# Performance work log

Hardware: AMD Instinct MI355X
Metric: run time of the kernel (lower is better)

The kernel has to match this reference:

```python
import jax, jax.numpy as jnp
import numpy as np

B, T, D, H = 8, 4096, 512, 512


def setup_inputs() -> dict:
    key = jax.random.key(0)
    k1, k2, k3, k4, k5, k6 = jax.random.split(key, 6)
    lim = 1.0 / np.sqrt(D)
    return {
        "x": jax.random.normal(k1, (B, T, D), dtype=jnp.float32),
        "h_0": jax.random.normal(k2, (B, 1, H), dtype=jnp.float32),
        "W_z": jax.random.uniform(k3, (H, D), jnp.float32, -lim, lim),
        "b_z": jax.random.uniform(k4, (H,), jnp.float32, -lim, lim),
        "W_h": jax.random.uniform(k5, (H, D), jnp.float32, -lim, lim),
        "b_h": jax.random.uniform(k6, (H,), jnp.float32, -lim, lim),
    }


def reference(x, h_0, W_z, b_z, W_h, b_h):
    # z_t = sigmoid(W_z x_t), h~_t = tanh(W_h x_t)
    z = jax.nn.sigmoid(jnp.einsum('btd,hd->bth', x, W_z) + b_z)  # (B,T,H)
    h_tilde = jnp.tanh(jnp.einsum('btd,hd->bth', x, W_h) + b_h)  # (B,T,H)
    a = 1.0 - z            # multiplicative coeffs
    b = z * h_tilde        # additive terms (b[:,0] handled as h0 carry)

    # linear recurrence h_t = a_t * h_{t-1} + b_t, h_0 given
    def scan_fn(h_prev, ab):
        a_t, b_t = ab
        h_t = a_t * h_prev + b_t
        return h_t, h_t

    a_t = jnp.swapaxes(a, 0, 1)  # (T,B,H)
    b_t = jnp.swapaxes(b, 0, 1)  # (T,B,H)
    _, hs = jax.lax.scan(scan_fn, h_0[:, 0, :], (a_t, b_t))
    return jnp.swapaxes(hs, 0, 1)  # (B,T,H)
```

## Files before the change

### kernel.cpp

```cpp
#include <hip/hip_runtime.h>

constexpr int Bn = 8, Tn = 4096, Dn = 512, Hn = 512;
constexpr int Mn = Bn * Tn;
constexpr int CH = 64, NC = Tn / CH;

typedef __attribute__((ext_vector_type(8))) short s8v;
typedef __attribute__((ext_vector_type(4))) float f4v;
typedef __attribute__((ext_vector_type(8))) _Float16 h8v;
typedef unsigned short ushort_t;

typedef __attribute__((address_space(1))) const void gv_t;
typedef __attribute__((address_space(3))) void lv_t;

__device__ __forceinline__ short f2bf(float f) {
  unsigned u = __float_as_uint(f);
  u = (u + 0x7fffu + ((u >> 16) & 1u)) >> 16;
  return (short)u;
}

__global__ __launch_bounds__(256) void convert_x(
    const float* __restrict__ X, ushort_t* __restrict__ Xb) {
  int lb = blockIdx.x, tid = threadIdx.x;
  const float* tsrc = X + ((size_t)(lb >> 4) * 128) * Dn + (lb & 15) * 32;
#pragma unroll
  for (int p = 0; p < 2; p++) {
    int idx = tid + p * 256;
    int r = idx >> 2, k8 = idx & 3;
    const float4* sv = reinterpret_cast<const float4*>(tsrc + (size_t)r * Dn + k8 * 8);
    float4 f0 = sv[0], f1 = sv[1];
    s8v v;
    v[0] = f2bf(f0.x); v[1] = f2bf(f0.y); v[2] = f2bf(f0.z); v[3] = f2bf(f0.w);
    v[4] = f2bf(f1.x); v[5] = f2bf(f1.y); v[6] = f2bf(f1.z); v[7] = f2bf(f1.w);
    int c = (r >> 4) * 64 + k8 * 16 + (r & 15);
    *reinterpret_cast<s8v*>(&Xb[((size_t)lb * 512 + c) * 8]) = v;
  }
}

__global__ __launch_bounds__(256) void convert_w(
    const float* __restrict__ Wz, const float* __restrict__ Wh,
    ushort_t* __restrict__ Wzb, ushort_t* __restrict__ Whb) {
  int bx = blockIdx.x, tid = threadIdx.x;
  const float* src;
  ushort_t* dst;
  int lb;
  if (bx < 64) { src = Wz; dst = Wzb; lb = bx; }
  else         { src = Wh; dst = Whb; lb = bx - 64; }
  const float* tsrc = src + ((size_t)(lb >> 4) * 128) * Dn + (lb & 15) * 32;
#pragma unroll
  for (int p = 0; p < 2; p++) {
    int idx = tid + p * 256;
    int r = idx >> 2, k8 = idx & 3;
    const float4* sv = reinterpret_cast<const float4*>(tsrc + (size_t)r * Dn + k8 * 8);
    float4 f0 = sv[0], f1 = sv[1];
    s8v v;
    v[0] = f2bf(f0.x); v[1] = f2bf(f0.y); v[2] = f2bf(f0.z); v[3] = f2bf(f0.w);
    v[4] = f2bf(f1.x); v[5] = f2bf(f1.y); v[6] = f2bf(f1.z); v[7] = f2bf(f1.w);
    int c = (r >> 4) * 64 + k8 * 16 + (r & 15);
    *reinterpret_cast<s8v*>(&dst[((size_t)lb * 512 + c) * 8]) = v;
  }
}

__global__ __launch_bounds__(512, 2) void gemm_act(
    const ushort_t* __restrict__ Xb, const ushort_t* __restrict__ Wzb,
    const ushort_t* __restrict__ Whb,
    const float* __restrict__ bzp, const float* __restrict__ bhp,
    h8v* __restrict__ cab, float* __restrict__ cA, float* __restrict__ cB) {
  __shared__ __align__(16) ushort_t lds[32 * 2048];

  int tid = threadIdx.x, lane = tid & 63, wid = tid >> 6;

  int o = blockIdx.x;
  int loc = o >> 3;
  int mt = (o & 7) * 8 + (loc >> 3);
  int p = loc & 7;

#pragma unroll
  for (int q = 0; q < 16; q++) {
    int r = q * 2 + (wid >> 2);
    int kt = r & 15;
    const ushort_t* wsrc = (r >= 16 ? Whb : Wzb);
    const ushort_t* s = wsrc + ((size_t)((p >> 1) * 16 + kt)) * 4096 + (p & 1) * 2048 + (tid & 255) * 8;
    __builtin_amdgcn_global_load_lds((gv_t*)s, (lv_t*)(lds + r * 2048 + (tid & 255) * 8), 16, 0, 0);
  }

  f4v accz[4][4], acch[4][4];
#pragma unroll
  for (int i = 0; i < 4; i++)
#pragma unroll
    for (int j = 0; j < 4; j++) {
      accz[i][j] = (f4v){0.f, 0.f, 0.f, 0.f};
      acch[i][j] = (f4v){0.f, 0.f, 0.f, 0.f};
    }

  int rw = mt * 8 + wid;
  int rt = rw >> 1, half = rw & 1;
  const ushort_t* xb = Xb + (size_t)rt * 16 * 4096;

  __syncthreads();

  auto ldW = [&](int kt, s8v* bzf, s8v* bhf) {
#pragma unroll
    for (int j = 0; j < 4; j++) {
      bzf[j] = *reinterpret_cast<const s8v*>(lds + (size_t)kt * 2048 + (j * 64 + lane) * 8);
      bhf[j] = *reinterpret_cast<const s8v*>(lds + (size_t)(16 + kt) * 2048 + (j * 64 + lane) * 8);
    }
  };
  auto mfmaStep = [&](s8v* af, s8v* bzf, s8v* bhf) {
    __builtin_amdgcn_s_setprio(1);
#pragma unroll
    for (int i = 0; i < 4; i++)
#pragma unroll
      for (int j = 0; j < 4; j++) {
        accz[i][j] = __builtin_amdgcn_mfma_f32_16x16x32_bf16(af[i], bzf[j], accz[i][j], 0, 0, 0);
        acch[i][j] = __builtin_amdgcn_mfma_f32_16x16x32_bf16(af[i], bhf[j], acch[i][j], 0, 0, 0);
      }
    __builtin_amdgcn_s_setprio(0);
  };

  s8v afA[4], afB[4];
#pragma unroll
  for (int i = 0; i < 4; i++)
    afA[i] = *reinterpret_cast<const s8v*>(xb + ((half * 4 + i) * 64 + lane) * 8);

#pragma unroll
  for (int kp = 0; kp < 8; kp++) {
    int k0 = 2 * kp;
#pragma unroll
    for (int i = 0; i < 4; i++)
      afB[i] = *reinterpret_cast<const s8v*>(xb + (size_t)(k0 + 1) * 4096 + ((half * 4 + i) * 64 + lane) * 8);
    s8v bz0[4], bh0[4];
    ldW(k0, bz0, bh0);
    mfmaStep(afA, bz0, bh0);
    if (k0 + 2 < 16) {
#pragma unroll
      for (int i = 0; i < 4; i++)
        afA[i] = *reinterpret_cast<const s8v*>(xb + (size_t)(k0 + 2) * 4096 + ((half * 4 + i) * 64 + lane) * 8);
    }
    s8v bz1[4], bh1[4];
    ldW(k0 + 1, bz1, bh1);
    mfmaStep(afB, bz1, bh1);
  }

  int R = rw, Cc = p;
  size_t base = (size_t)(R * 8 + Cc) * 1024;
  float bzv[4], bhv[4];
#pragma unroll
  for (int j = 0; j < 4; j++) {
    int h = p * 64 + j * 16 + (lane & 15);
    bzv[j] = bzp[h];
    bhv[j] = bhp[h];
  }
  float QA[4][4], QB[4][4];
#pragma unroll
  for (int i = 0; i < 4; i++)
#pragma unroll
    for (int j = 0; j < 4; j++) {
      h8v g;
      float Pa = 1.f, Pb = 0.f;
#pragma unroll
      for (int q = 0; q < 4; q++) {
        float z = 1.f / (1.f + __expf(-(accz[i][j][q] + bzv[j])));
        float e = __expf(2.f * (acch[i][j][q] + bhv[j]));
        float th = 1.f - 2.f / (e + 1.f);
        g[q] = (_Float16)(1.f - z);
        g[4 + q] = (_Float16)(z * th);
        float a = (float)g[q], b = (float)g[4 + q];
        Pa = a * Pa;
        Pb = a * Pb + b;
      }
      cab[base + (size_t)((i * 4 + j) * 64 + lane)] = g;
      QA[i][j] = Pa;
      QB[i][j] = Pb;
    }

#pragma unroll
  for (int j = 0; j < 4; j++) {
    float A = 1.f, Bv = 0.f;
#pragma unroll
    for (int i = 0; i < 4; i++) {
      float a = QA[i][j], b = QB[i][j];
      float ap = __shfl_xor(a, 16), bp = __shfl_xor(b, 16);
      bool hi = (lane & 16) != 0;
      float af_ = hi ? ap : a, bf_ = hi ? bp : b;
      float as_ = hi ? a : ap, bs_ = hi ? b : bp;
      a = as_ * af_; b = as_ * bf_ + bs_;
      ap = __shfl_xor(a, 32); bp = __shfl_xor(b, 32);
      bool hi2 = (lane & 32) != 0;
      af_ = hi2 ? ap : a; bf_ = hi2 ? bp : b;
      as_ = hi2 ? a : ap; bs_ = hi2 ? b : bp;
      a = as_ * af_; b = as_ * bf_ + bs_;
      Bv = a * Bv + b;
      A = a * A;
    }
    if (lane < 16) {
      int h = p * 64 + j * 16 + lane;
      cA[(size_t)R * Hn + h] = A;
      cB[(size_t)R * Hn + h] = Bv;
    }
  }
}

__global__ __launch_bounds__(256) void scan_heads(
    const float* __restrict__ cA, const float* __restrict__ cB,
    const float* __restrict__ h0p, float* __restrict__ hst) {
  int gid = blockIdx.x * 256 + threadIdx.x;
  int b = gid >> 9, h = gid & 511;
  float hr = h0p[(size_t)b * Hn + h];
#pragma unroll 8
  for (int c = 0; c < NC; c++) {
    size_t o = (size_t)(b * NC + c) * Hn + h;
    hst[o] = hr;
    hr = fmaf(cA[o], hr, cB[o]);
  }
}

__global__ __launch_bounds__(256) void scan_apply(
    const h8v* __restrict__ cab, const float* __restrict__ hst,
    float* __restrict__ out) {
  int h = blockIdx.y * 256 + threadIdx.x;
  int R = blockIdx.x;
  int hl = h & 63, Cc = h >> 6;
  size_t base = (size_t)(R * 8 + Cc) * 1024 + (size_t)(hl >> 4) * 64 + (hl & 15);
  float hr = hst[(size_t)R * Hn + h];
  size_t ob = (size_t)R * 64 * Hn + h;
#pragma unroll
  for (int i = 0; i < 4; i++)
#pragma unroll
    for (int p = 0; p < 4; p++) {
      h8v g = cab[base + i * 256 + p * 16];
#pragma unroll
      for (int q = 0; q < 4; q++) {
        hr = fmaf((float)g[q], hr, (float)g[4 + q]);
        out[ob + (size_t)(i * 16 + p * 4 + q) * Hn] = hr;
      }
    }
}

extern "C" void kernel_launch(void* const* d_in, const int* in_sizes, int n_in,
                              void* d_out, int out_size, void* d_ws, size_t ws_size,
                              hipStream_t stream) {
  const float* X   = (const float*)d_in[0];
  const float* h0p = (const float*)d_in[1];
  const float* Wz  = (const float*)d_in[2];
  const float* bz  = (const float*)d_in[3];
  const float* Wh  = (const float*)d_in[4];
  const float* bh  = (const float*)d_in[5];
  float* out = (float*)d_out;

  char* ws = (char*)d_ws;
  ushort_t* Xb  = (ushort_t*)ws;
  ushort_t* Wzb = Xb + (size_t)Mn * Dn;
  ushort_t* Whb = Wzb + (size_t)Hn * Dn;
  h8v* cab      = (h8v*)(Whb + (size_t)Hn * Dn);
  float* cA     = (float*)(cab + (size_t)Mn * Hn / 4);
  float* cB     = cA + (size_t)Bn * NC * Hn;
  float* hst    = cB + (size_t)Bn * NC * Hn;

  convert_x<<<dim3(4096), 256, 0, stream>>>(X, Xb);
  convert_w<<<dim3(128), 256, 0, stream>>>(Wz, Wh, Wzb, Whb);

  gemm_act<<<dim3(512), 512, 0, stream>>>(Xb, Wzb, Whb, bz, bh, cab, cA, cB);

  scan_heads<<<dim3(Bn * Hn / 256), 256, 0, stream>>>(cA, cB, h0p, hst);
  scan_apply<<<dim3(Mn / 64, Hn / 256), 256, 0, stream>>>(cab, hst, out);
}
```

Measured before the change: 95.66 us.

## Fuse x bf16 conversion into GEMM and loop two M-tiles per block

Removes the separate convert_x pass and its bf16 workspace. The GEMM now reads fp32 x straight from global memory and converts it to bf16 in registers with v_cvt_pk_bf16_f32. Each block loops over two M tiles so the W tiles loaded into LDS are reused twice, which halves the grid to 256 blocks. The trade-off is that the GEMM reads twice as many bytes of x per fragment, and with 256 blocks of 512 threads at launch_bounds 2 per CU, occupancy is roughly one block per CU.

```diff
diff --git a/kernel.cpp b/kernel.cpp
--- a/kernel.cpp
+++ b/kernel.cpp
@@ -16,24 +16,6 @@
   unsigned u = __float_as_uint(f);
   u = (u + 0x7fffu + ((u >> 16) & 1u)) >> 16;
   return (short)u;
-}
-
-__global__ __launch_bounds__(256) void convert_x(
-    const float* __restrict__ X, ushort_t* __restrict__ Xb) {
-  int lb = blockIdx.x, tid = threadIdx.x;
-  const float* tsrc = X + ((size_t)(lb >> 4) * 128) * Dn + (lb & 15) * 32;
-#pragma unroll
-  for (int p = 0; p < 2; p++) {
-    int idx = tid + p * 256;
-    int r = idx >> 2, k8 = idx & 3;
-    const float4* sv = reinterpret_cast<const float4*>(tsrc + (size_t)r * Dn + k8 * 8);
-    float4 f0 = sv[0], f1 = sv[1];
-    s8v v;
-    v[0] = f2bf(f0.x); v[1] = f2bf(f0.y); v[2] = f2bf(f0.z); v[3] = f2bf(f0.w);
-    v[4] = f2bf(f1.x); v[5] = f2bf(f1.y); v[6] = f2bf(f1.z); v[7] = f2bf(f1.w);
-    int c = (r >> 4) * 64 + k8 * 16 + (r & 15);
-    *reinterpret_cast<s8v*>(&Xb[((size_t)lb * 512 + c) * 8]) = v;
-  }
 }
 
 __global__ __launch_bounds__(256) void convert_w(
@@ -61,18 +43,16 @@
 }
 
 __global__ __launch_bounds__(512, 2) void gemm_act(
-    const ushort_t* __restrict__ Xb, const ushort_t* __restrict__ Wzb,
+    const float* __restrict__ X, const ushort_t* __restrict__ Wzb,
     const ushort_t* __restrict__ Whb,
     const float* __restrict__ bzp, const float* __restrict__ bhp,
     h8v* __restrict__ cab, float* __restrict__ cA, float* __restrict__ cB) {
   __shared__ __align__(16) ushort_t lds[32 * 2048];
 
   int tid = threadIdx.x, lane = tid & 63, wid = tid >> 6;
-
   int o = blockIdx.x;
-  int loc = o >> 3;
-  int mt = (o & 7) * 8 + (loc >> 3);
-  int p = loc & 7;
+  int p = o & 7;
+  int mtp = o >> 3;
 
 #pragma unroll
   for (int q = 0; q < 16; q++) {
@@ -82,20 +62,6 @@
     const ushort_t* s = wsrc + ((size_t)((p >> 1) * 16 + kt)) * 4096 + (p & 1) * 2048 + (tid & 255) * 8;
     __builtin_amdgcn_global_load_lds((gv_t*)s, (lv_t*)(lds + r * 2048 + (tid & 255) * 8), 16, 0, 0);
   }
-
-  f4v accz[4][4], acch[4][4];
-#pragma unroll
-  for (int i = 0; i < 4; i++)
-#pragma unroll
-    for (int j = 0; j < 4; j++) {
-      accz[i][j] = (f4v){0.f, 0.f, 0.f, 0.f};
-      acch[i][j] = (f4v){0.f, 0.f, 0.f, 0.f};
-    }
-
-  int rw = mt * 8 + wid;
-  int rt = rw >> 1, half = rw & 1;
-  const ushort_t* xb = Xb + (size_t)rt * 16 * 4096;
-
   __syncthreads();
 
   auto ldW = [&](int kt, s8v* bzf, s8v* bhf) {
@@ -105,97 +71,115 @@
       bhf[j] = *reinterpret_cast<const s8v*>(lds + (size_t)(16 + kt) * 2048 + (j * 64 + lane) * 8);
     }
   };
-  auto mfmaStep = [&](s8v* af, s8v* bzf, s8v* bhf) {
-    __builtin_amdgcn_s_setprio(1);
+  auto cvtFrag = [&](const float4& a, const float4& b) -> s8v {
+    union { unsigned u[4]; s8v v; } r;
+    asm("v_cvt_pk_bf16_f32 %0, %1, %2" : "=v"(r.u[0]) : "v"(a.x), "v"(a.y));
+    asm("v_cvt_pk_bf16_f32 %0, %1, %2" : "=v"(r.u[1]) : "v"(a.z), "v"(a.w));
+    asm("v_cvt_pk_bf16_f32 %0, %1, %2" : "=v"(r.u[2]) : "v"(b.x), "v"(b.y));
+    asm("v_cvt_pk_bf16_f32 %0, %1, %2" : "=v"(r.u[3]) : "v"(b.z), "v"(b.w));
+    return r.v;
+  };
+
+  for (int m2 = 0; m2 < 2; m2++) {
+    int mt = mtp * 2 + m2;
+    int rw = mt * 8 + wid;
+    const float* Xp = X + (size_t)(rw * 64 + (lane & 15)) * Dn + (lane >> 4) * 8;
+
+    auto loadX = [&](int kt, float4* xf) {
+#pragma unroll
+      for (int i = 0; i < 4; i++) {
+        const float4* si = reinterpret_cast<const float4*>(Xp + (size_t)i * 16 * Dn + kt * 32);
+        xf[2 * i] = si[0];
+        xf[2 * i + 1] = si[1];
+      }
+    };
+
+    f4v accz[4][4], acch[4][4];
 #pragma unroll
     for (int i = 0; i < 4; i++)
 #pragma unroll
       for (int j = 0; j < 4; j++) {
-        accz[i][j] = __builtin_amdgcn_mfma_f32_16x16x32_bf16(af[i], bzf[j], accz[i][j], 0, 0, 0);
-        acch[i][j] = __builtin_amdgcn_mfma_f32_16x16x32_bf16(af[i], bhf[j], acch[i][j], 0, 0, 0);
-      }
-    __builtin_amdgcn_s_setprio(0);
-  };
-
-  s8v afA[4], afB[4];
-#pragma unroll
-  for (int i = 0; i < 4; i++)
-    afA[i] = *reinterpret_cast<const s8v*>(xb + ((half * 4 + i) * 64 + lane) * 8);
-
-#pragma unroll
-  for (int kp = 0; kp < 8; kp++) {
-    int k0 = 2 * kp;
+        accz[i][j] = (f4v){0.f, 0.f, 0.f, 0.f};
+        acch[i][j] = (f4v){0.f, 0.f, 0.f, 0.f};
+      }
+
+    float4 xf[8];
+    loadX(0, xf);
+#pragma unroll
+    for (int kt = 0; kt < 16; kt++) {
+      s8v af[4];
+#pragma unroll
+      for (int i = 0; i < 4; i++) af[i] = cvtFrag(xf[2 * i], xf[2 * i + 1]);
+      if (kt < 15) loadX(kt + 1, xf);
+      s8v bzf[4], bhf[4];
+      ldW(kt, bzf, bhf);
+      __builtin_amdgcn_s_setprio(1);
+#pragma unroll
+      for (int i = 0; i < 4; i++)
+#pragma unroll
+        for (int j = 0; j < 4; j++) {
+          accz[i][j] = __builtin_amdgcn_mfma_f32_16x16x32_bf16(af[i], bzf[j], accz[i][j], 0, 0, 0);
+          acch[i][j] = __builtin_amdgcn_mfma_f32_16x16x32_bf16(af[i], bhf[j], acch[i][j], 0, 0, 0);
+        }
+      __builtin_amdgcn_s_setprio(0);
+    }
+
+    int R = rw, Cc = p;
+    size_t base = (size_t)(R * 8 + Cc) * 1024;
+    float bzv[4], bhv[4];
+#pragma unroll
+    for (int j = 0; j < 4; j++) {
+      int h = p * 64 + j * 16 + (lane & 15);
+      bzv[j] = bzp[h];
+      bhv[j] = bhp[h];
+    }
+    float QA[4][4], QB[4][4];
 #pragma unroll
     for (int i = 0; i < 4; i++)
-      afB[i] = *reinterpret_cast<const s8v*>(xb + (size_t)(k0 + 1) * 4096 + ((half * 4 + i) * 64 + lane) * 8);
-    s8v bz0[4], bh0[4];
-    ldW(k0, bz0, bh0);
-    mfmaStep(afA, bz0, bh0);
-    if (k0 + 2 < 16) {
-#pragma unroll
-      for (int i = 0; i < 4; i++)
-        afA[i] = *reinterpret_cast<const s8v*>(xb + (size_t)(k0 + 2) * 4096 + ((half * 4 + i) * 64 + lane) * 8);
-    }
-    s8v bz1[4], bh1[4];
-    ldW(k0 + 1, bz1, bh1);
-    mfmaStep(afB, bz1, bh1);
-  }
-
-  int R = rw, Cc = p;
-  size_t base = (size_t)(R * 8 + Cc) * 1024;
-  float bzv[4], bhv[4];
-#pragma unroll
-  for (int j = 0; j < 4; j++) {
-    int h = p * 64 + j * 16 + (lane & 15);
-    bzv[j] = bzp[h];
-    bhv[j] = bhp[h];
-  }
-  float QA[4][4], QB[4][4];
-#pragma unroll
-  for (int i = 0; i < 4; i++)
+#pragma unroll
+      for (int j = 0; j < 4; j++) {
+        h8v g;
+        float Pa = 1.f, Pb = 0.f;
+#pragma unroll
+        for (int q = 0; q < 4; q++) {
+          float z = 1.f / (1.f + __expf(-(accz[i][j][q] + bzv[j])));
+          float e = __expf(2.f * (acch[i][j][q] + bhv[j]));
+          float th = 1.f - 2.f / (e + 1.f);
+          g[q] = (_Float16)(1.f - z);
+          g[4 + q] = (_Float16)(z * th);
+          float a = (float)g[q], b = (float)g[4 + q];
+          Pa = a * Pa;
+          Pb = a * Pb + b;
+        }
+        cab[base + (size_t)((i * 4 + j) * 64 + lane)] = g;
+        QA[i][j] = Pa;
+        QB[i][j] = Pb;
+      }
+
 #pragma unroll
     for (int j = 0; j < 4; j++) {
-      h8v g;
-      float Pa = 1.f, Pb = 0.f;
-#pragma unroll
-      for (int q = 0; q < 4; q++) {
-        float z = 1.f / (1.f + __expf(-(accz[i][j][q] + bzv[j])));
-        float e = __expf(2.f * (acch[i][j][q] + bhv[j]));
-        float th = 1.f - 2.f / (e + 1.f);
-        g[q] = (_Float16)(1.f - z);
-        g[4 + q] = (_Float16)(z * th);
-        float a = (float)g[q], b = (float)g[4 + q];
-        Pa = a * Pa;
-        Pb = a * Pb + b;
-      }
-      cab[base + (size_t)((i * 4 + j) * 64 + lane)] = g;
-      QA[i][j] = Pa;
-      QB[i][j] = Pb;
-    }
-
-#pragma unroll
-  for (int j = 0; j < 4; j++) {
-    float A = 1.f, Bv = 0.f;
-#pragma unroll
-    for (int i = 0; i < 4; i++) {
-      float a = QA[i][j], b = QB[i][j];
-      float ap = __shfl_xor(a, 16), bp = __shfl_xor(b, 16);
-      bool hi = (lane & 16) != 0;
-      float af_ = hi ? ap : a, bf_ = hi ? bp : b;
-      float as_ = hi ? a : ap, bs_ = hi ? b : bp;
-      a = as_ * af_; b = as_ * bf_ + bs_;
-      ap = __shfl_xor(a, 32); bp = __shfl_xor(b, 32);
-      bool hi2 = (lane & 32) != 0;
-      af_ = hi2 ? ap : a; bf_ = hi2 ? bp : b;
-      as_ = hi2 ? a : ap; bs_ = hi2 ? b : bp;
-      a = as_ * af_; b = as_ * bf_ + bs_;
-      Bv = a * Bv + b;
-      A = a * A;
-    }
-    if (lane < 16) {
-      int h = p * 64 + j * 16 + lane;
-      cA[(size_t)R * Hn + h] = A;
-      cB[(size_t)R * Hn + h] = Bv;
+      float A = 1.f, Bv = 0.f;
+#pragma unroll
+      for (int i = 0; i < 4; i++) {
+        float a = QA[i][j], b = QB[i][j];
+        float ap = __shfl_xor(a, 16), bp = __shfl_xor(b, 16);
+        bool hi = (lane & 16) != 0;
+        float af_ = hi ? ap : a, bf_ = hi ? bp : b;
+        float as_ = hi ? a : ap, bs_ = hi ? b : bp;
+        a = as_ * af_; b = as_ * bf_ + bs_;
+        ap = __shfl_xor(a, 32); bp = __shfl_xor(b, 32);
+        bool hi2 = (lane & 32) != 0;
+        af_ = hi2 ? ap : a; bf_ = hi2 ? bp : b;
+        as_ = hi2 ? a : ap; bs_ = hi2 ? b : bp;
+        a = as_ * af_; b = as_ * bf_ + bs_;
+        Bv = a * Bv + b;
+        A = a * A;
+      }
+      if (lane < 16) {
+        int h = p * 64 + j * 16 + lane;
+        cA[(size_t)R * Hn + h] = A;
+        cB[(size_t)R * Hn + h] = Bv;
+      }
     }
   }
 }
@@ -248,18 +232,16 @@
   float* out = (float*)d_out;
 
   char* ws = (char*)d_ws;
-  ushort_t* Xb  = (ushort_t*)ws;
-  ushort_t* Wzb = Xb + (size_t)Mn * Dn;
+  ushort_t* Wzb = (ushort_t*)ws;
   ushort_t* Whb = Wzb + (size_t)Hn * Dn;
   h8v* cab      = (h8v*)(Whb + (size_t)Hn * Dn);
   float* cA     = (float*)(cab + (size_t)Mn * Hn / 4);
   float* cB     = cA + (size_t)Bn * NC * Hn;
   float* hst    = cB + (size_t)Bn * NC * Hn;
 
-  convert_x<<<dim3(4096), 256, 0, stream>>>(X, Xb);
   convert_w<<<dim3(128), 256, 0, stream>>>(Wz, Wh, Wzb, Whb);
 
-  gemm_act<<<dim3(512), 512, 0, stream>>>(Xb, Wzb, Whb, bz, bh, cab, cA, cB);
+  gemm_act<<<dim3(256), 512, 0, stream>>>(X, Wzb, Whb, bz, bh, cab, cA, cB);
 
   scan_heads<<<dim3(Bn * Hn / 256), 256, 0, stream>>>(cA, cB, h0p, hst);
   scan_apply<<<dim3(Mn / 64, Hn / 256), 256, 0, stream>>>(cab, hst, out);
```

Measured after the change: 134.3 us. 40.4% more time.

## Split GEMM block across 16 waves, halving per-wave N tile

Applied to the files above, without the earlier changes.

Grows the gemm_act block from 8 to 16 waves. Each pair of waves now shares a 64-row M strip and splits the 64 columns into two 32-column halves, which cuts per-wave accumulators from 32 to 16 MFMA tiles and lowers register pressure. W staging into LDS is spread over 1024 threads and the s_setprio hints are removed. Each X fragment is now loaded from global twice (once per column-half wave), so global X traffic doubles. That extra traffic is traded for more waves in flight to hide latency.

```diff
diff --git a/kernel.cpp b/kernel.cpp
--- a/kernel.cpp
+++ b/kernel.cpp
@@ -60,107 +60,100 @@
   }
 }
 
-__global__ __launch_bounds__(512, 2) void gemm_act(
+__global__ __launch_bounds__(1024, 4) void gemm_act(
     const ushort_t* __restrict__ Xb, const ushort_t* __restrict__ Wzb,
     const ushort_t* __restrict__ Whb,
     const float* __restrict__ bzp, const float* __restrict__ bhp,
     h8v* __restrict__ cab, float* __restrict__ cA, float* __restrict__ cB) {
-  __shared__ __align__(16) ushort_t lds[32 * 2048];
+  __shared__ __align__(16) ushort_t lds[65536];
 
   int tid = threadIdx.x, lane = tid & 63, wid = tid >> 6;
+  int wr = wid >> 1, wc = wid & 1;
 
   int o = blockIdx.x;
   int loc = o >> 3;
   int mt = (o & 7) * 8 + (loc >> 3);
   int p = loc & 7;
 
-#pragma unroll
-  for (int q = 0; q < 16; q++) {
-    int r = q * 2 + (wid >> 2);
-    int kt = r & 15;
-    const ushort_t* wsrc = (r >= 16 ? Whb : Wzb);
-    const ushort_t* s = wsrc + ((size_t)((p >> 1) * 16 + kt)) * 4096 + (p & 1) * 2048 + (tid & 255) * 8;
-    __builtin_amdgcn_global_load_lds((gv_t*)s, (lv_t*)(lds + r * 2048 + (tid & 255) * 8), 16, 0, 0);
-  }
-
-  f4v accz[4][4], acch[4][4];
+  const ushort_t* wzp = Wzb + ((size_t)(p >> 1) * 16) * 4096 + (p & 1) * 2048;
+  const ushort_t* whp = Whb + ((size_t)(p >> 1) * 16) * 4096 + (p & 1) * 2048;
+#pragma unroll
+  for (int q = 0; q < 8; q++) {
+    int idx = q * 1024 + tid;
+    int r = idx >> 8, cc = idx & 255;
+    const ushort_t* src = (r < 16 ? wzp + (size_t)r * 4096
+                                  : whp + (size_t)(r - 16) * 4096) + cc * 8;
+    __builtin_amdgcn_global_load_lds((gv_t*)src, (lv_t*)(lds + idx * 8), 16, 0, 0);
+  }
+
+  f4v accz[4][2], acch[4][2];
 #pragma unroll
   for (int i = 0; i < 4; i++)
 #pragma unroll
-    for (int j = 0; j < 4; j++) {
-      accz[i][j] = (f4v){0.f, 0.f, 0.f, 0.f};
-      acch[i][j] = (f4v){0.f, 0.f, 0.f, 0.f};
-    }
-
-  int rw = mt * 8 + wid;
+    for (int jj = 0; jj < 2; jj++) {
+      accz[i][jj] = (f4v){0.f, 0.f, 0.f, 0.f};
+      acch[i][jj] = (f4v){0.f, 0.f, 0.f, 0.f};
+    }
+
+  int rw = mt * 8 + wr;
   int rt = rw >> 1, half = rw & 1;
-  const ushort_t* xb = Xb + (size_t)rt * 16 * 4096;
+  const s8v* xs = reinterpret_cast<const s8v*>(Xb) + (size_t)rt * 16 * 512 + (half * 4) * 64 + lane;
+  const ushort_t* lz = lds;
+  const ushort_t* lh = lds + 32768;
+  int cb0 = (wc * 2) * 64 + lane;
 
   __syncthreads();
 
-  auto ldW = [&](int kt, s8v* bzf, s8v* bhf) {
-#pragma unroll
-    for (int j = 0; j < 4; j++) {
-      bzf[j] = *reinterpret_cast<const s8v*>(lds + (size_t)kt * 2048 + (j * 64 + lane) * 8);
-      bhf[j] = *reinterpret_cast<const s8v*>(lds + (size_t)(16 + kt) * 2048 + (j * 64 + lane) * 8);
-    }
+  auto ldX = [&](s8v* A, int kt) {
+#pragma unroll
+    for (int i = 0; i < 4; i++) A[i] = xs[kt * 512 + i * 64];
   };
-  auto mfmaStep = [&](s8v* af, s8v* bzf, s8v* bhf) {
-    __builtin_amdgcn_s_setprio(1);
+  auto step = [&](int kt, s8v* A) {
+    s8v bz[2], bh[2];
+#pragma unroll
+    for (int jj = 0; jj < 2; jj++) {
+      bz[jj] = *reinterpret_cast<const s8v*>(lz + (size_t)kt * 2048 + (size_t)(cb0 + jj * 64) * 8);
+      bh[jj] = *reinterpret_cast<const s8v*>(lh + (size_t)kt * 2048 + (size_t)(cb0 + jj * 64) * 8);
+    }
 #pragma unroll
     for (int i = 0; i < 4; i++)
 #pragma unroll
-      for (int j = 0; j < 4; j++) {
-        accz[i][j] = __builtin_amdgcn_mfma_f32_16x16x32_bf16(af[i], bzf[j], accz[i][j], 0, 0, 0);
-        acch[i][j] = __builtin_amdgcn_mfma_f32_16x16x32_bf16(af[i], bhf[j], acch[i][j], 0, 0, 0);
+      for (int jj = 0; jj < 2; jj++) {
+        accz[i][jj] = __builtin_amdgcn_mfma_f32_16x16x32_bf16(A[i], bz[jj], accz[i][jj], 0, 0, 0);
+        acch[i][jj] = __builtin_amdgcn_mfma_f32_16x16x32_bf16(A[i], bh[jj], acch[i][jj], 0, 0, 0);
       }
-    __builtin_amdgcn_s_setprio(0);
   };
 
-  s8v afA[4], afB[4];
-#pragma unroll
-  for (int i = 0; i < 4; i++)
-    afA[i] = *reinterpret_cast<const s8v*>(xb + ((half * 4 + i) * 64 + lane) * 8);
-
+  s8v A0[4], A1[4];
+  ldX(A0, 0); ldX(A1, 1);
 #pragma unroll
   for (int kp = 0; kp < 8; kp++) {
-    int k0 = 2 * kp;
-#pragma unroll
-    for (int i = 0; i < 4; i++)
-      afB[i] = *reinterpret_cast<const s8v*>(xb + (size_t)(k0 + 1) * 4096 + ((half * 4 + i) * 64 + lane) * 8);
-    s8v bz0[4], bh0[4];
-    ldW(k0, bz0, bh0);
-    mfmaStep(afA, bz0, bh0);
-    if (k0 + 2 < 16) {
-#pragma unroll
-      for (int i = 0; i < 4; i++)
-        afA[i] = *reinterpret_cast<const s8v*>(xb + (size_t)(k0 + 2) * 4096 + ((half * 4 + i) * 64 + lane) * 8);
-    }
-    s8v bz1[4], bh1[4];
-    ldW(k0 + 1, bz1, bh1);
-    mfmaStep(afB, bz1, bh1);
+    step(2 * kp, A0);
+    if (kp < 7) ldX(A0, 2 * kp + 2);
+    step(2 * kp + 1, A1);
+    if (kp < 7) ldX(A1, 2 * kp + 3);
   }
 
   int R = rw, Cc = p;
   size_t base = (size_t)(R * 8 + Cc) * 1024;
-  float bzv[4], bhv[4];
-#pragma unroll
-  for (int j = 0; j < 4; j++) {
-    int h = p * 64 + j * 16 + (lane & 15);
-    bzv[j] = bzp[h];
-    bhv[j] = bhp[h];
-  }
-  float QA[4][4], QB[4][4];
+  float bzv[2], bhv[2];
+#pragma unroll
+  for (int jj = 0; jj < 2; jj++) {
+    int h = p * 64 + (wc * 2 + jj) * 16 + (lane & 15);
+    bzv[jj] = bzp[h];
+    bhv[jj] = bhp[h];
+  }
+  float QA[4][2], QB[4][2];
 #pragma unroll
   for (int i = 0; i < 4; i++)
 #pragma unroll
-    for (int j = 0; j < 4; j++) {
+    for (int jj = 0; jj < 2; jj++) {
       h8v g;
       float Pa = 1.f, Pb = 0.f;
 #pragma unroll
       for (int q = 0; q < 4; q++) {
-        float z = 1.f / (1.f + __expf(-(accz[i][j][q] + bzv[j])));
-        float e = __expf(2.f * (acch[i][j][q] + bhv[j]));
+        float z = 1.f / (1.f + __expf(-(accz[i][jj][q] + bzv[jj])));
+        float e = __expf(2.f * (acch[i][jj][q] + bhv[jj]));
         float th = 1.f - 2.f / (e + 1.f);
         g[q] = (_Float16)(1.f - z);
         g[4 + q] = (_Float16)(z * th);
@@ -168,17 +161,17 @@
         Pa = a * Pa;
         Pb = a * Pb + b;
       }
-      cab[base + (size_t)((i * 4 + j) * 64 + lane)] = g;
-      QA[i][j] = Pa;
-      QB[i][j] = Pb;
-    }
-
-#pragma unroll
-  for (int j = 0; j < 4; j++) {
+      cab[base + (size_t)((i * 4 + wc * 2 + jj) * 64 + lane)] = g;
+      QA[i][jj] = Pa;
+      QB[i][jj] = Pb;
+    }
+
+#pragma unroll
+  for (int jj = 0; jj < 2; jj++) {
     float A = 1.f, Bv = 0.f;
 #pragma unroll
     for (int i = 0; i < 4; i++) {
-      float a = QA[i][j], b = QB[i][j];
+      float a = QA[i][jj], b = QB[i][jj];
       float ap = __shfl_xor(a, 16), bp = __shfl_xor(b, 16);
       bool hi = (lane & 16) != 0;
       float af_ = hi ? ap : a, bf_ = hi ? bp : b;
@@ -193,7 +186,7 @@
       A = a * A;
     }
     if (lane < 16) {
-      int h = p * 64 + j * 16 + lane;
+      int h = p * 64 + (wc * 2 + jj) * 16 + lane;
       cA[(size_t)R * Hn + h] = A;
       cB[(size_t)R * Hn + h] = Bv;
     }
@@ -259,7 +252,7 @@
   convert_x<<<dim3(4096), 256, 0, stream>>>(X, Xb);
   convert_w<<<dim3(128), 256, 0, stream>>>(Wz, Wh, Wzb, Whb);
 
-  gemm_act<<<dim3(512), 512, 0, stream>>>(Xb, Wzb, Whb, bz, bh, cab, cA, cB);
+  gemm_act<<<dim3(512), 1024, 0, stream>>>(Xb, Wzb, Whb, bz, bh, cab, cA, cB);
 
   scan_heads<<<dim3(Bn * Hn / 256), 256, 0, stream>>>(cA, cB, h0p, hst);
   scan_apply<<<dim3(Mn / 64, Hn / 256), 256, 0, stream>>>(cab, hst, out);
```

Result: slower. 101.8 us (+6.4%).

## Restructure gemm_act into a double-buffered LDS-staged 2D block tiling

Applied to the files above, without the earlier changes.

The fused gate GEMM now tiles each workgroup as a 256-row by 128-column block and stages both X and W tiles through LDS. Staging uses double-buffered global_load_lds, with explicit waitcnt and barriers so the next K-step loads while the current one runs MFMAs. Previously each wave streamed its own X rows straight from global memory and only W was cached in LDS. Each wave now computes either the z or the h projection for a 128x64 sub-tile, and the partner results are swapped through LDS before the activation and chunk-scan epilogue. The aim is better reuse of X and W and more overlap of loads with compute, at the cost of extra barriers and an LDS exchange of accumulators.

```diff
diff --git a/kernel.cpp b/kernel.cpp
--- a/kernel.cpp
+++ b/kernel.cpp
@@ -65,88 +65,121 @@
     const ushort_t* __restrict__ Whb,
     const float* __restrict__ bzp, const float* __restrict__ bhp,
     h8v* __restrict__ cab, float* __restrict__ cA, float* __restrict__ cB) {
-  __shared__ __align__(16) ushort_t lds[32 * 2048];
+  __shared__ __align__(16) ushort_t lds[65536];
 
   int tid = threadIdx.x, lane = tid & 63, wid = tid >> 6;
+  int wr = wid >> 2;
+  int wc = wid & 3;
+  int is_h = wc >> 1, c01 = wc & 1;
 
   int o = blockIdx.x;
-  int loc = o >> 3;
-  int mt = (o & 7) * 8 + (loc >> 3);
-  int p = loc & 7;
-
-#pragma unroll
-  for (int q = 0; q < 16; q++) {
-    int r = q * 2 + (wid >> 2);
-    int kt = r & 15;
-    const ushort_t* wsrc = (r >= 16 ? Whb : Wzb);
-    const ushort_t* s = wsrc + ((size_t)((p >> 1) * 16 + kt)) * 4096 + (p & 1) * 2048 + (tid & 255) * 8;
-    __builtin_amdgcn_global_load_lds((gv_t*)s, (lv_t*)(lds + r * 2048 + (tid & 255) * 8), 16, 0, 0);
-  }
-
-  f4v accz[4][4], acch[4][4];
-#pragma unroll
-  for (int i = 0; i < 4; i++)
-#pragma unroll
-    for (int j = 0; j < 4; j++) {
-      accz[i][j] = (f4v){0.f, 0.f, 0.f, 0.f};
-      acch[i][j] = (f4v){0.f, 0.f, 0.f, 0.f};
-    }
-
-  int rw = mt * 8 + wid;
-  int rt = rw >> 1, half = rw & 1;
-  const ushort_t* xb = Xb + (size_t)rt * 16 * 4096;
+  int wg = (o & 7) * 64 + (o >> 3);
+  int bm = wg >> 2;
+  int bh = wg & 3;
+
+  auto stageHalf = [&](int b, int ks, int half) {
+    int k2 = half >> 1;
+    int kt = ks * 2 + k2;
+    if ((half & 1) == 0) {
+#pragma unroll
+      for (int r2 = 0; r2 < 2; r2++) {
+        const ushort_t* s = Xb + ((size_t)((bm * 2 + r2) * 16 + kt)) * 4096 + tid * 8;
+        __builtin_amdgcn_global_load_lds(
+            (gv_t*)s, (lv_t*)(lds + b * 16384 + (k2 * 2 + r2) * 4096 + tid * 8), 16, 0, 0);
+      }
+    } else {
+#pragma unroll
+      for (int m = 0; m < 2; m++) {
+        const ushort_t* s = (m ? Whb : Wzb) + ((size_t)(bh * 16 + kt)) * 4096 + tid * 8;
+        __builtin_amdgcn_global_load_lds(
+            (gv_t*)s, (lv_t*)(lds + 32768 + b * 16384 + (k2 * 2 + m) * 4096 + tid * 8), 16, 0, 0);
+      }
+    }
+  };
+
+  f4v acc[8][4];
+#pragma unroll
+  for (int i = 0; i < 8; i++)
+#pragma unroll
+    for (int j = 0; j < 4; j++) acc[i][j] = (f4v){0.f, 0.f, 0.f, 0.f};
+
+#pragma unroll
+  for (int h = 0; h < 4; h++) stageHalf(0, 0, h);
+
+  int cur = 0;
+  for (int ks = 0; ks < 8; ks++) {
+    s8v Bf[4];
+#pragma unroll
+    for (int q = 0; q < 4; q++) {
+      constexpr int K2[4] = {0, 0, 1, 1};
+      constexpr int IH[4] = {0, 1, 0, 1};
+      int k2 = K2[q];
+      if (q == 0) {
+        asm volatile("s_waitcnt vmcnt(4)" ::: "memory");
+        __builtin_amdgcn_sched_barrier(0);
+        __builtin_amdgcn_s_barrier();
+      } else if (q == 2) {
+        if (ks == 7) asm volatile("s_waitcnt vmcnt(0)" ::: "memory");
+        else         asm volatile("s_waitcnt vmcnt(4)" ::: "memory");
+        __builtin_amdgcn_sched_barrier(0);
+        __builtin_amdgcn_s_barrier();
+      }
+      s8v Af[4];
+#pragma unroll
+      for (int ii = 0; ii < 4; ii++) {
+        int g = IH[q] * 4 + ii;
+        Af[ii] = *reinterpret_cast<const s8v*>(
+            lds + cur * 16384 + (k2 * 2 + wr) * 4096 + (g * 64 + lane) * 8);
+      }
+      if (IH[q] == 0) {
+#pragma unroll
+        for (int j = 0; j < 4; j++) {
+          int gj = c01 * 4 + j;
+          Bf[j] = *reinterpret_cast<const s8v*>(
+              lds + 32768 + cur * 16384 + (k2 * 2 + is_h) * 4096 + (gj * 64 + lane) * 8);
+        }
+      }
+      if (ks + 1 < 8) stageHalf(cur ^ 1, ks + 1, q);
+      asm volatile("s_waitcnt lgkmcnt(0)" ::: "memory");
+      __builtin_amdgcn_sched_barrier(0);
+      __builtin_amdgcn_s_setprio(1);
+#pragma unroll
+      for (int ii = 0; ii < 4; ii++)
+#pragma unroll
+        for (int j = 0; j < 4; j++)
+          acc[IH[q] * 4 + ii][j] =
+              __builtin_amdgcn_mfma_f32_16x16x32_bf16(Af[ii], Bf[j], acc[IH[q] * 4 + ii][j], 0, 0, 0);
+      __builtin_amdgcn_s_setprio(0);
+      __builtin_amdgcn_sched_barrier(0);
+      __builtin_amdgcn_s_barrier();
+    }
+    cur ^= 1;
+  }
 
   __syncthreads();
-
-  auto ldW = [&](int kt, s8v* bzf, s8v* bhf) {
-#pragma unroll
-    for (int j = 0; j < 4; j++) {
-      bzf[j] = *reinterpret_cast<const s8v*>(lds + (size_t)kt * 2048 + (j * 64 + lane) * 8);
-      bhf[j] = *reinterpret_cast<const s8v*>(lds + (size_t)(16 + kt) * 2048 + (j * 64 + lane) * 8);
-    }
-  };
-  auto mfmaStep = [&](s8v* af, s8v* bzf, s8v* bhf) {
-    __builtin_amdgcn_s_setprio(1);
+  f4v* ex = reinterpret_cast<f4v*>(lds);
+  size_t slot = (size_t)wid * 1024;
+  if (!is_h) {
 #pragma unroll
     for (int i = 0; i < 4; i++)
 #pragma unroll
-      for (int j = 0; j < 4; j++) {
-        accz[i][j] = __builtin_amdgcn_mfma_f32_16x16x32_bf16(af[i], bzf[j], accz[i][j], 0, 0, 0);
-        acch[i][j] = __builtin_amdgcn_mfma_f32_16x16x32_bf16(af[i], bhf[j], acch[i][j], 0, 0, 0);
-      }
-    __builtin_amdgcn_s_setprio(0);
-  };
-
-  s8v afA[4], afB[4];
-#pragma unroll
-  for (int i = 0; i < 4; i++)
-    afA[i] = *reinterpret_cast<const s8v*>(xb + ((half * 4 + i) * 64 + lane) * 8);
-
-#pragma unroll
-  for (int kp = 0; kp < 8; kp++) {
-    int k0 = 2 * kp;
+      for (int j = 0; j < 4; j++) ex[slot + (i * 4 + j) * 64 + lane] = acc[i + 4][j];
+  } else {
 #pragma unroll
     for (int i = 0; i < 4; i++)
-      afB[i] = *reinterpret_cast<const s8v*>(xb + (size_t)(k0 + 1) * 4096 + ((half * 4 + i) * 64 + lane) * 8);
-    s8v bz0[4], bh0[4];
-    ldW(k0, bz0, bh0);
-    mfmaStep(afA, bz0, bh0);
-    if (k0 + 2 < 16) {
-#pragma unroll
-      for (int i = 0; i < 4; i++)
-        afA[i] = *reinterpret_cast<const s8v*>(xb + (size_t)(k0 + 2) * 4096 + ((half * 4 + i) * 64 + lane) * 8);
-    }
-    s8v bz1[4], bh1[4];
-    ldW(k0 + 1, bz1, bh1);
-    mfmaStep(afB, bz1, bh1);
-  }
-
-  int R = rw, Cc = p;
+#pragma unroll
+      for (int j = 0; j < 4; j++) ex[slot + (i * 4 + j) * 64 + lane] = acc[i][j];
+  }
+  __syncthreads();
+  size_t pslot = (size_t)(wid ^ 2) * 1024;
+
+  int R = bm * 4 + wr * 2 + is_h;
+  int Cc = bh * 2 + c01;
   size_t base = (size_t)(R * 8 + Cc) * 1024;
   float bzv[4], bhv[4];
 #pragma unroll
   for (int j = 0; j < 4; j++) {
-    int h = p * 64 + j * 16 + (lane & 15);
+    int h = bh * 128 + c01 * 64 + j * 16 + (lane & 15);
     bzv[j] = bzp[h];
     bhv[j] = bhp[h];
   }
@@ -155,12 +188,16 @@
   for (int i = 0; i < 4; i++)
 #pragma unroll
     for (int j = 0; j < 4; j++) {
+      f4v other = ex[pslot + (i * 4 + j) * 64 + lane];
+      f4v vz4, vh4;
+      if (!is_h) { vz4 = acc[i][j]; vh4 = other; }
+      else       { vz4 = other;     vh4 = acc[i + 4][j]; }
       h8v g;
       float Pa = 1.f, Pb = 0.f;
 #pragma unroll
       for (int q = 0; q < 4; q++) {
-        float z = 1.f / (1.f + __expf(-(accz[i][j][q] + bzv[j])));
-        float e = __expf(2.f * (acch[i][j][q] + bhv[j]));
+        float z = 1.f / (1.f + __expf(-(vz4[q] + bzv[j])));
+        float e = __expf(2.f * (vh4[q] + bhv[j]));
         float th = 1.f - 2.f / (e + 1.f);
         g[q] = (_Float16)(1.f - z);
         g[4 + q] = (_Float16)(z * th);
@@ -193,7 +230,7 @@
       A = a * A;
     }
     if (lane < 16) {
-      int h = p * 64 + j * 16 + lane;
+      int h = bh * 128 + c01 * 64 + j * 16 + lane;
       cA[(size_t)R * Hn + h] = A;
       cB[(size_t)R * Hn + h] = Bv;
     }
```

Result: slower. 99.76 us (+4.3%).
